# Performance work log

Measured on AMD Instinct MI355X. Metric: run time of the kernel, lower is better.

The kernel has to match this reference:

```python
import jax, jax.numpy as jnp
import numpy as np
from jax import lax

CURRICULUM_EP = 12
LI, LS, LW = 0.5, 0.8, 3.0


def _gauss_win(ws, C, dtype):
    coords = jnp.arange(ws, dtype=jnp.float32) - ws // 2
    g = jnp.exp(-coords ** 2 / (2 * 1.5 ** 2))
    win = g[None, :] * g[:, None]
    win = win / win.sum()
    # depthwise kernel, OIHW with I=1, O=C
    return jnp.broadcast_to(win[None, None], (C, 1, ws, ws)).astype(dtype)


def _dwconv(x, win, p, C):
    return lax.conv_general_dilated(
        x, win, window_strides=(1, 1), padding=[(p, p), (p, p)],
        dimension_numbers=('NCHW', 'OIHW', 'NCHW'), feature_group_count=C)


def diff_ssim(x, y, ws=11):
    C1, C2 = 0.01 ** 2, 0.03 ** 2
    C = x.shape[1]
    p = ws // 2
    win = _gauss_win(ws, C, x.dtype)
    mx = _dwconv(x, win, p, C)
    my = _dwconv(y, win, p, C)
    sxx = _dwconv(x * x, win, p, C) - mx ** 2
    syy = _dwconv(y * y, win, p, C) - my ** 2
    sxy = _dwconv(x * y, win, p, C) - mx * my
    ssim_map = (2 * mx * my + C1) * (2 * sxy + C2) / ((mx ** 2 + my ** 2 + C1) * (sxx + syy + C2))
    return ssim_map.mean()


def setup_inputs() -> dict:
    key = jax.random.key(0)
    k1, k2, k3, k4 = jax.random.split(key, 4)
    B, C, H, W = 16, 3, 512, 512
    NB = 1024  # watermark bits
    eps = 1e-4
    cover = jax.random.uniform(k1, (B, C, H, W), dtype=jnp.float32)
    wmed = jax.random.uniform(k2, (B, C, H, W), dtype=jnp.float32)
    wm_orig = jax.random.uniform(k3, (B, NB), dtype=jnp.float32)
    wm_ext = jnp.clip(jax.random.uniform(k4, (B, NB), dtype=jnp.float32), eps, 1.0 - eps)
    return {"cover": cover, "wmed": wmed, "wm_orig": wm_orig, "wm_ext": wm_ext, "epoch": 20}


def reference(cover, wmed, wm_orig, wm_ext, epoch):
    ml = jnp.mean((wmed - cover) ** 2)
    sv = diff_ssim(wmed, cover)
    sl = 1.0 - sv
    wl = jnp.mean(-(wm_orig * jnp.log(wm_ext) + (1.0 - wm_orig) * jnp.log(1.0 - wm_ext)))
    if epoch <= CURRICULUM_EP:
        w_img, w_ssim = 0.05, 0.05
    else:
        progress = min(1.0, (epoch - CURRICULUM_EP) / 10.0)
        w_img = 0.05 + (LI - 0.05) * progress
        w_ssim = 0.05 + (LS - 0.05) * progress
    total = w_img * ml + w_ssim * sl + LW * wl
    return (total, ml, sv, wl)
```

## Files before the change

### kernel.cpp

```cpp
#include <hip/hip_runtime.h>
#include <math.h>

#define H_IMG 512
#define W_IMG 512
#define TH 32
#define TW 32
#define HALO 5
#define WS11 11
#define SH (TH + 2*HALO)
#define NTHREADS 256
#define TPB 4

#define RWF 33
#define RWR (5*RWF)
#define RBUF_N (SH*RWR)

#define W0 0.00102838f
#define W1 0.00759873f
#define W2 0.03600075f
#define W3 0.10936070f
#define W4 0.21300556f
#define W5 0.26601172f
__device__ __constant__ float c_w[WS11] = {W0,W1,W2,W3,W4,W5,W4,W3,W2,W1,W0};

__global__ __launch_bounds__(NTHREADS, 5) void ssim_mse_tile(
        const float* __restrict__ cover, const float* __restrict__ wmed,
        float* __restrict__ part, int nParts) {
    __shared__ __align__(16) float rbuf[RBUF_N];
    __shared__ float red[8];

    const int tid = threadIdx.x;
    float ssim_acc = 0.f, mse_acc = 0.f;

    for (int it = 0; it < TPB; ++it) {
        const int tile = blockIdx.x * TPB + it;
        const int bx = tile & 15;
        const int by = (tile >> 4) & 15;
        const int pl = tile >> 8;
        const size_t pbase = (size_t)pl * (H_IMG*W_IMG);
        const float* xp = wmed + pbase;
        const float* yp = cover + pbase;
        const int ty0 = by*TH - HALO;
        const int tx0 = bx*TW - HALO;
        const bool xin = (bx != 0) && (bx != 15);

        for (int t = tid; t < SH*8; t += NTHREADS) {
            const int r = t >> 3, c0 = (t & 7) << 2;
            const int gy = ty0 + r;
            const bool rok = (unsigned)gy < (unsigned)H_IMG;
            float xv[14], yv[14];
            if (rok && xin) {
                const int ga = tx0 + c0 - 3;
                const float* rx = xp + (size_t)gy*W_IMG + ga;
                const float* ry = yp + (size_t)gy*W_IMG + ga;
                float4 XA = *(const float4*)(rx);
                float4 XB = *(const float4*)(rx + 4);
                float4 XC = *(const float4*)(rx + 8);
                float4 XD = *(const float4*)(rx + 12);
                float  XE = rx[16];
                float4 YA = *(const float4*)(ry);
                float4 YB = *(const float4*)(ry + 4);
                float4 YC = *(const float4*)(ry + 8);
                float4 YD = *(const float4*)(ry + 12);
                float  YE = ry[16];
                xv[0]=XA.w;  xv[1]=XB.x;  xv[2]=XB.y;  xv[3]=XB.z;  xv[4]=XB.w;
                xv[5]=XC.x;  xv[6]=XC.y;  xv[7]=XC.z;  xv[8]=XC.w;  xv[9]=XD.x;
                xv[10]=XD.y; xv[11]=XD.z; xv[12]=XD.w; xv[13]=XE;
                yv[0]=YA.w;  yv[1]=YB.x;  yv[2]=YB.y;  yv[3]=YB.z;  yv[4]=YB.w;
                yv[5]=YC.x;  yv[6]=YC.y;  yv[7]=YC.z;  yv[8]=YC.w;  yv[9]=YD.x;
                yv[10]=YD.y; yv[11]=YD.z; yv[12]=YD.w; yv[13]=YE;
            } else if (rok) {
                const int gc = tx0 + c0;
                const float* prx = xp + (size_t)gy*W_IMG + gc;
                const float* pry = yp + (size_t)gy*W_IMG + gc;
#pragma unroll
                for (int j = 0; j < 14; ++j) {
                    bool ok = (unsigned)(gc + j) < (unsigned)W_IMG;
                    xv[j] = ok ? prx[j] : 0.f;
                    yv[j] = ok ? pry[j] : 0.f;
                }
            } else {
#pragma unroll
                for (int j = 0; j < 14; ++j) { xv[j] = 0.f; yv[j] = 0.f; }
            }

            if (rok && r >= HALO && r < HALO+TH) {
#pragma unroll
                for (int j = 5; j < 9; ++j) {
                    float d = xv[j] - yv[j];
                    mse_acc = fmaf(d, d, mse_acc);
                }
            }

            float a0[4]={0,0,0,0}, a1[4]={0,0,0,0}, a2[4]={0,0,0,0};
            float a3[4]={0,0,0,0}, a4[4]={0,0,0,0};
#pragma unroll
            for (int j = 0; j < 14; ++j) {
                float px = xv[j], py = yv[j];
                float pxx = px*px, pyy = py*py, pxy = px*py;
#pragma unroll
                for (int k = 0; k < 4; ++k) {
                    int tap = j - k;
                    if (tap >= 0 && tap < WS11) {
                        float wv = c_w[tap];
                        a0[k] = fmaf(wv, px,  a0[k]);
                        a1[k] = fmaf(wv, py,  a1[k]);
                        a2[k] = fmaf(wv, pxx, a2[k]);
                        a3[k] = fmaf(wv, pyy, a3[k]);
                        a4[k] = fmaf(wv, pxy, a4[k]);
                    }
                }
            }
            float* wb = &rbuf[r*RWR + c0];
#pragma unroll
            for (int k = 0; k < 4; ++k) {
                wb[0*RWF + k] = a0[k];
                wb[1*RWF + k] = a1[k];
                wb[2*RWF + k] = a2[k];
                wb[3*RWF + k] = a3[k];
                wb[4*RWF + k] = a4[k];
            }
        }
        __syncthreads();

        {
            const float C1 = 0.01f*0.01f, C2 = 0.03f*0.03f;
            const int c  = tid & 31;
            const int r0 = (tid >> 5) << 2;
            float m0[4]={0,0,0,0}, m1[4]={0,0,0,0}, e2[4]={0,0,0,0};
            float e3[4]={0,0,0,0}, e4[4]={0,0,0,0};
#pragma unroll
            for (int i = 0; i < 14; ++i) {
                const float* rb = &rbuf[(r0 + i)*RWR + c];
                float v0 = rb[0*RWF], v1 = rb[1*RWF], v2 = rb[2*RWF];
                float v3 = rb[3*RWF], v4 = rb[4*RWF];
#pragma unroll
                for (int k = 0; k < 4; ++k) {
                    int tap = i - k;
                    if (tap >= 0 && tap < WS11) {
                        float wv = c_w[tap];
                        m0[k] = fmaf(wv, v0, m0[k]);
                        m1[k] = fmaf(wv, v1, m1[k]);
                        e2[k] = fmaf(wv, v2, e2[k]);
                        e3[k] = fmaf(wv, v3, e3[k]);
                        e4[k] = fmaf(wv, v4, e4[k]);
                    }
                }
            }
#pragma unroll
            for (int k = 0; k < 4; ++k) {
                float mx = m0[k], my = m1[k];
                float sxx = e2[k] - mx*mx;
                float syy = e3[k] - my*my;
                float sxy = e4[k] - mx*my;
                float num = (2.f*mx*my + C1) * (2.f*sxy + C2);
                float den = (mx*mx + my*my + C1) * (sxx + syy + C2);
                ssim_acc += __fdividef(num, den);
            }
        }
        __syncthreads();
    }

#pragma unroll
    for (int off = 32; off > 0; off >>= 1) {
        ssim_acc += __shfl_down(ssim_acc, off);
        mse_acc  += __shfl_down(mse_acc, off);
    }
    int wid = tid >> 6, lane = tid & 63;
    if (lane == 0) { red[wid] = ssim_acc; red[4+wid] = mse_acc; }
    __syncthreads();
    if (tid == 0) {
        float s = red[0]+red[1]+red[2]+red[3];
        float m = red[4]+red[5]+red[6]+red[7];
        part[blockIdx.x] = s;
        part[nParts + blockIdx.x] = m;
    }
}

#define FT 1024
__global__ __launch_bounds__(FT) void finalize_k(
        const float* __restrict__ part, int nParts,
        const float* __restrict__ wm_orig, const float* __restrict__ wm_ext,
        int nWm, const int* __restrict__ epoch_p,
        float* __restrict__ out, double inv_npix, double inv_nwm) {
    __shared__ double red[48];
    int tid = threadIdx.x;
    double s_ssim = 0.0, s_mse = 0.0, s_wl = 0.0;
    const float4* s4 = (const float4*)part;
    const float4* m4 = (const float4*)(part + nParts);
    int n4 = nParts >> 2;
    for (int i = tid; i < n4; i += FT) {
        float4 v = s4[i];
        s_ssim += (double)((v.x + v.y) + (v.z + v.w));
        float4 u = m4[i];
        s_mse  += (double)((u.x + u.y) + (u.z + u.w));
    }
    const float4* p4 = (const float4*)wm_orig;
    const float4* q4 = (const float4*)wm_ext;
    int w4 = nWm >> 2;
    for (int i = tid; i < w4; i += FT) {
        float4 p = p4[i], q = q4[i];
        float a;
        a  = -(p.x*__logf(q.x) + (1.f-p.x)*__logf(1.f-q.x));
        a += -(p.y*__logf(q.y) + (1.f-p.y)*__logf(1.f-q.y));
        a += -(p.z*__logf(q.z) + (1.f-p.z)*__logf(1.f-q.z));
        a += -(p.w*__logf(q.w) + (1.f-p.w)*__logf(1.f-q.w));
        s_wl += (double)a;
    }
#pragma unroll
    for (int off = 32; off > 0; off >>= 1) {
        s_ssim += __shfl_down(s_ssim, off);
        s_mse  += __shfl_down(s_mse, off);
        s_wl   += __shfl_down(s_wl, off);
    }
    int wid = tid >> 6, lane = tid & 63;
    if (lane == 0) { red[wid] = s_ssim; red[16+wid] = s_mse; red[32+wid] = s_wl; }
    __syncthreads();
    if (tid == 0) {
        double ssim_sum = 0.0, mse_sum = 0.0, wl_sum = 0.0;
        for (int i = 0; i < 16; ++i) {
            ssim_sum += red[i]; mse_sum += red[16+i]; wl_sum += red[32+i];
        }
        float sv = (float)(ssim_sum * inv_npix);
        float ml = (float)(mse_sum  * inv_npix);
        float wl = (float)(wl_sum   * inv_nwm);
        int e = *epoch_p;
        float w_img, w_ssim;
        if (e <= 12) {
            w_img = 0.05f; w_ssim = 0.05f;
        } else {
            float progress = fminf(1.0f, (float)(e - 12) / 10.0f);
            w_img  = 0.05f + (0.5f - 0.05f)*progress;
            w_ssim = 0.05f + (0.8f - 0.05f)*progress;
        }
        float sl = 1.0f - sv;
        float total = w_img*ml + w_ssim*sl + 3.0f*wl;
        out[0] = total;
        out[1] = ml;
        out[2] = sv;
        out[3] = wl;
    }
}

extern "C" void kernel_launch(void* const* d_in, const int* in_sizes, int n_in,
                              void* d_out, int out_size, void* d_ws, size_t ws_size,
                              hipStream_t stream) {
    const float* cover   = (const float*)d_in[0];
    const float* wmed    = (const float*)d_in[1];
    const float* wm_orig = (const float*)d_in[2];
    const float* wm_ext  = (const float*)d_in[3];
    const int*   epoch   = (const int*)d_in[4];
    float* out = (float*)d_out;

    int npix   = in_sizes[0];
    int planes = npix / (H_IMG * W_IMG);
    int nWm    = in_sizes[2];

    int nTiles  = 16 * 16 * planes;
    int nBlocks = nTiles / TPB;
    int nParts  = nBlocks;
    float* part = (float*)d_ws;

    ssim_mse_tile<<<nBlocks, NTHREADS, 0, stream>>>(cover, wmed, part, nParts);
    finalize_k<<<1, FT, 0, stream>>>(part, nParts, wm_orig, wm_ext, nWm,
                                     epoch, out,
                                     1.0 / (double)npix, 1.0 / (double)nWm);
}
```

Before: 198.5 us.

## Use planar shared layout, float4 stores and 8-row vertical register blocking

Shared memory changes from interleaved per-row fields to five planar field arrays with a padded stride, so the horizontal pass can write with float4 stores. The vertical pass now has each thread compute 8 output rows from 18 loads instead of 4 rows from 14, which cuts shared-memory reads per output. Only half the block does the vertical pass, alternating halves by tile parity, so half the warps sit idle during that phase. Launch bounds drop to 4 blocks per SM to make room for the larger accumulator set.

```diff
diff --git a/kernel.cpp b/kernel.cpp
--- a/kernel.cpp
+++ b/kernel.cpp
@@ -11,9 +11,8 @@
 #define NTHREADS 256
 #define TPB 4
 
-#define RWF 33
-#define RWR (5*RWF)
-#define RBUF_N (SH*RWR)
+#define RS 36
+#define RBUF_N (5*SH*RS)
 
 #define W0 0.00102838f
 #define W1 0.00759873f
@@ -23,7 +22,7 @@
 #define W5 0.26601172f
 __device__ __constant__ float c_w[WS11] = {W0,W1,W2,W3,W4,W5,W4,W3,W2,W1,W0};
 
-__global__ __launch_bounds__(NTHREADS, 5) void ssim_mse_tile(
+__global__ __launch_bounds__(NTHREADS, 4) void ssim_mse_tile(
         const float* __restrict__ cover, const float* __restrict__ wmed,
         float* __restrict__ part, int nParts) {
     __shared__ __align__(16) float rbuf[RBUF_N];
@@ -111,48 +110,45 @@
                     }
                 }
             }
-            float* wb = &rbuf[r*RWR + c0];
-#pragma unroll
-            for (int k = 0; k < 4; ++k) {
-                wb[0*RWF + k] = a0[k];
-                wb[1*RWF + k] = a1[k];
-                wb[2*RWF + k] = a2[k];
-                wb[3*RWF + k] = a3[k];
-                wb[4*RWF + k] = a4[k];
-            }
+            float* wb = &rbuf[r*RS + c0];
+            *(float4*)(wb + 0*SH*RS) = make_float4(a0[0],a0[1],a0[2],a0[3]);
+            *(float4*)(wb + 1*SH*RS) = make_float4(a1[0],a1[1],a1[2],a1[3]);
+            *(float4*)(wb + 2*SH*RS) = make_float4(a2[0],a2[1],a2[2],a2[3]);
+            *(float4*)(wb + 3*SH*RS) = make_float4(a3[0],a3[1],a3[2],a3[3]);
+            *(float4*)(wb + 4*SH*RS) = make_float4(a4[0],a4[1],a4[2],a4[3]);
         }
         __syncthreads();
 
-        {
+        if (((tid >> 7) & 1) == (it & 1)) {
             const float C1 = 0.01f*0.01f, C2 = 0.03f*0.03f;
-            const int c  = tid & 31;
-            const int r0 = (tid >> 5) << 2;
-            float m0[4]={0,0,0,0}, m1[4]={0,0,0,0}, e2[4]={0,0,0,0};
-            float e3[4]={0,0,0,0}, e4[4]={0,0,0,0};
-#pragma unroll
-            for (int i = 0; i < 14; ++i) {
-                const float* rb = &rbuf[(r0 + i)*RWR + c];
-                float v0 = rb[0*RWF], v1 = rb[1*RWF], v2 = rb[2*RWF];
-                float v3 = rb[3*RWF], v4 = rb[4*RWF];
-#pragma unroll
-                for (int k = 0; k < 4; ++k) {
-                    int tap = i - k;
-                    if (tap >= 0 && tap < WS11) {
-                        float wv = c_w[tap];
-                        m0[k] = fmaf(wv, v0, m0[k]);
-                        m1[k] = fmaf(wv, v1, m1[k]);
-                        e2[k] = fmaf(wv, v2, e2[k]);
-                        e3[k] = fmaf(wv, v3, e3[k]);
-                        e4[k] = fmaf(wv, v4, e4[k]);
+            const int s  = tid & 127;
+            const int c  = s & 31;
+            const int r0 = (s >> 5) << 3;
+            float acc[5][8];
+#pragma unroll
+            for (int f = 0; f < 5; ++f)
+#pragma unroll
+                for (int k = 0; k < 8; ++k) acc[f][k] = 0.f;
+#pragma unroll
+            for (int f = 0; f < 5; ++f) {
+                const float* rb = &rbuf[f*SH*RS + r0*RS + c];
+#pragma unroll
+                for (int i = 0; i < 18; ++i) {
+                    float v = rb[i*RS];
+#pragma unroll
+                    for (int k = 0; k < 8; ++k) {
+                        int tap = i - k;
+                        if (tap >= 0 && tap < WS11)
+                            acc[f][k] = fmaf(c_w[tap], v, acc[f][k]);
                     }
                 }
             }
 #pragma unroll
-            for (int k = 0; k < 4; ++k) {
-                float mx = m0[k], my = m1[k];
-                float sxx = e2[k] - mx*mx;
-                float syy = e3[k] - my*my;
-                float sxy = e4[k] - mx*my;
+            for (int k = 0; k < 8; ++k) {
+                float mx = acc[0][k], my = acc[1][k];
+                float sxx = acc[2][k] - mx*mx;
+                float syy = acc[3][k] - my*my;
+                float sxy = acc[4][k] - mx*my;
                 float num = (2.f*mx*my + C1) * (2.f*sxy + C2);
                 float den = (mx*mx + my*my + C1) * (sxx + syy + C2);
                 ssim_acc += __fdividef(num, den);
```

New measurement: 198.4 us. Within noise of the previous version (-0.0%).
